# Kernel optimization log

Measured on AMD Instinct MI355X. Metric: run time of the kernel, lower is better.

Reference implementation:

```python
import jax, jax.numpy as jnp
import numpy as np

K = 3          # kernel_size
STRIDE = 1
PAD = 1
DIL = 1


def setup_inputs() -> dict:
    key = jax.random.key(0)
    k1, k2, k3, k4, k5 = jax.random.split(key, 5)
    x = jax.random.normal(k1, (4, 64, 128, 128), jnp.float32)
    weight = jax.random.normal(k2, (64, 64, K, K), jnp.float32) * 0.05   # [O, C, K, K]
    bias = jax.random.normal(k3, (64,), jnp.float32) * 0.05
    # offset conv params: small nonzero so offsets actually exercise bilinear sampling
    offset_w = jax.random.normal(k4, (2 * K * K, 64, K, K), jnp.float32) * 0.01
    offset_b = jax.random.normal(k5, (2 * K * K,), jnp.float32) * 0.1
    return {"x": x, "weight": weight, "bias": bias,
            "offset_w": offset_w, "offset_b": offset_b}


def _conv2d(x, w, b):
    y = jax.lax.conv_general_dilated(
        x, w, window_strides=(STRIDE, STRIDE),
        padding=((PAD, PAD), (PAD, PAD)), rhs_dilation=(DIL, DIL),
        dimension_numbers=("NCHW", "OIHW", "NCHW"))
    return y + b[None, :, None, None]


def _bilinear_sample(img, ys, xs):
    # img: [C, H, W]; ys, xs: [KK, Ho, Wo] float sampling coords
    H, W = img.shape[1], img.shape[2]
    y0 = jnp.floor(ys)
    x0 = jnp.floor(xs)
    y1 = y0 + 1.0
    x1 = x0 + 1.0
    wy1 = ys - y0
    wx1 = xs - x0
    wy0 = 1.0 - wy1
    wx0 = 1.0 - wx1

    def gather(yy, xx):
        valid = (yy >= 0) & (yy <= H - 1) & (xx >= 0) & (xx <= W - 1)
        yi = jnp.clip(yy, 0, H - 1).astype(jnp.int32)
        xi = jnp.clip(xx, 0, W - 1).astype(jnp.int32)
        v = img[:, yi, xi]                     # [C, KK, Ho, Wo]
        return v * valid.astype(img.dtype)

    return (gather(y0, x0) * (wy0 * wx0) + gather(y0, x1) * (wy0 * wx1)
            + gather(y1, x0) * (wy1 * wx0) + gather(y1, x1) * (wy1 * wx1))


def reference(x, weight, bias, offset_w, offset_b):
    B, C, H, W = x.shape
    KK = K * K
    # offsets: [B, 2*K*K, Ho, Wo], per-location (dy, dx) for each kernel tap
    offset = _conv2d(x, offset_w, offset_b)
    Ho, Wo = offset.shape[2], offset.shape[3]
    off = offset.reshape(B, KK, 2, Ho, Wo)
    dy, dx = off[:, :, 0], off[:, :, 1]        # [B, KK, Ho, Wo]

    ki, kj = jnp.meshgrid(jnp.arange(K), jnp.arange(K), indexing="ij")
    ki = ki.reshape(KK).astype(x.dtype)
    kj = kj.reshape(KK).astype(x.dtype)
    oy = (jnp.arange(Ho) * STRIDE - PAD).astype(x.dtype)
    ox = (jnp.arange(Wo) * STRIDE - PAD).astype(x.dtype)
    base_y = oy[None, :, None] + (ki * DIL)[:, None, None]   # [KK, Ho, 1]
    base_x = ox[None, None, :] + (kj * DIL)[:, None, None]   # [KK, 1, Wo]
    ys = base_y[None] + dy                                   # [B, KK, Ho, Wo]
    xs = base_x[None] + dx

    # sampled: [B, C, KK, Ho, Wo]
    sampled = jax.vmap(_bilinear_sample)(x, ys, xs)
    w = weight.reshape(weight.shape[0], C, KK)
    out = jnp.einsum("bckhw,ock->bohw", sampled, w) + bias[None, :, None, None]
    return out
```

## Files before the change

kernel.cpp:

```cpp
#include <hip/hip_runtime.h>
#include <hip/hip_bf16.h>

#define B_ 4
#define C_ 64
#define H_ 128
#define W_ 128
#define HW_ (H_ * W_)
#define OCH_ 18

typedef __attribute__((ext_vector_type(8))) short short8;
typedef __attribute__((ext_vector_type(16))) float f32x16;

#define W2B_ELEMS (9 * 2 * 4 * 64 * 8)
#define W2A_ELEMS (36 * 64 * 8)

#define PSTRIDE_B (6 * 128 * 16 + 16)
#define SMEM_BYTES (8 * PSTRIDE_B)

__device__ __forceinline__ unsigned short f2bf(float f) {
  union { float f; unsigned u; } v; v.f = f;
  unsigned r = v.u + 0x7FFFu + ((v.u >> 16) & 1u);
  return (unsigned short)(r >> 16);
}
__device__ __forceinline__ float bf2f(unsigned short h) {
  union { unsigned u; float f; } v; v.u = ((unsigned)h) << 16;
  return v.f;
}
__device__ __forceinline__ unsigned short f2bfh(float f) {
  __hip_bfloat16 h = __float2bfloat16(f);
  return *reinterpret_cast<unsigned short*>(&h);
}
__device__ __forceinline__ int swz256(int x) { return (x & 7) * 32 + (x >> 3); }
__device__ __forceinline__ int swe(int row, int col) {
  int e = (row << 7) + col;
  e ^= (col >> 3) & 7;
  return e << 4;
}

__global__ __launch_bounds__(256) void pack_w_only(
    const float* __restrict__ wmain, const float* __restrict__ offw,
    unsigned short* __restrict__ ws_u) {
  int idx = blockIdx.x * 256 + threadIdx.x;
  if (idx < W2B_ELEMS) {
    int i = idx & 7, lane = (idx >> 3) & 63, s = (idx >> 9) & 3;
    int mq = (idx >> 11) & 1, t = idx >> 12;
    int o = mq * 32 + (lane & 31);
    int c = 16 * s + (lane >> 5) * 8 + i;
    ws_u[idx] = f2bf(wmain[(o * 64 + c) * 9 + t]);
  } else if (idx < W2B_ELEMS + W2A_ELEMS) {
    int j = idx - W2B_ELEMS;
    int i = j & 7, lane = (j >> 3) & 63, s = j >> 9;
    int kg = 16 * s + (lane >> 5) * 8 + i;
    int t = kg >> 6, c = kg & 63, oc = lane & 31;
    ws_u[idx] = (oc < OCH_) ? f2bf(offw[(oc * 64 + c) * 9 + t]) : (unsigned short)0;
  }
}

template<int KI, int KJ>
__device__ __forceinline__ void tap_full(
    float dy, float dx, int ho, int ho0, int px, int lane, int b,
    const char* __restrict__ win, const float* __restrict__ x,
    const unsigned short* __restrict__ wt2,
    f32x16& acc0, f32x16& acc1) {
  const float ys = (float)(ho - 1 + KI) + dy;
  const float xs = (float)(px - 1 + KJ) + dx;
  const float y0f = floorf(ys), x0f = floorf(xs);
  const int y0 = (int)y0f, x0 = (int)x0f;
  const int y1 = y0 + 1, x1 = x0 + 1;
  const float wy1 = ys - y0f, wx1 = xs - x0f;
  const float wy0 = 1.f - wy1, wx0 = 1.f - wx1;
  const bool vy0 = (unsigned)y0 < (unsigned)H_, vy1 = (unsigned)y1 < (unsigned)H_;
  const bool vx0 = (unsigned)x0 < (unsigned)W_, vx1 = (unsigned)x1 < (unsigned)W_;
  const float g00 = (vy0 && vx0) ? wy0 * wx0 : 0.f;
  const float g01 = (vy0 && vx1) ? wy0 * wx1 : 0.f;
  const float g10 = (vy1 && vx0) ? wy1 * wx0 : 0.f;
  const float g11 = (vy1 && vx1) ? wy1 * wx1 : 0.f;
  const int yc0 = min(max(y0, 0), H_ - 1), yc1 = min(max(y1, 0), H_ - 1);
  const int xc0 = min(max(x0, 0), W_ - 1), xc1 = min(max(x1, 0), W_ - 1);
  const int rr0 = yc0 - ho0 + 2, rr1 = yc1 - ho0 + 2;
  const bool in = ((unsigned)rr0 < 6u) & ((unsigned)rr1 < 6u);
  const int laneh = lane >> 5;

  if (__builtin_expect(__any(!in), 0)) {
    const float* xb = x + (size_t)b * C_ * HW_;
    #pragma unroll 1
    for (int ss = 0; ss < 4; ++ss) {
      short8 bf;
      #pragma unroll
      for (int i = 0; i < 8; ++i) {
        const float* img = xb + (size_t)((2 * ss + laneh) * 8 + i) * HW_;
        float v = g00 * img[yc0 * W_ + xc0] + g01 * img[yc0 * W_ + xc1]
                + g10 * img[yc1 * W_ + xc0] + g11 * img[yc1 * W_ + xc1];
        bf[i] = (short)f2bfh(v);
      }
      const short8 a0 = *(const short8*)&wt2[(ss * 64 + lane) * 8];
      const short8 a1 = *(const short8*)&wt2[((4 + ss) * 64 + lane) * 8];
      acc0 = __builtin_amdgcn_mfma_f32_32x32x16_bf16(a0, bf, acc0, 0, 0, 0);
      acc1 = __builtin_amdgcn_mfma_f32_32x32x16_bf16(a1, bf, acc1, 0, 0, 0);
    }
    return;
  }

  const int u00 = swe(rr0, xc0), u01 = swe(rr0, xc1);
  const int u10 = swe(rr1, xc0), u11 = swe(rr1, xc1);
  #pragma unroll
  for (int ss = 0; ss < 4; ++ss) {
    const char* pb = win + (2 * ss + laneh) * PSTRIDE_B;
    short8 c00 = *(const short8*)(pb + u00);
    short8 c01 = *(const short8*)(pb + u01);
    short8 c10 = *(const short8*)(pb + u10);
    short8 c11 = *(const short8*)(pb + u11);
    short8 bf;
    #pragma unroll
    for (int i = 0; i < 8; ++i) {
      float v = g00 * bf2f((unsigned short)c00[i]) + g01 * bf2f((unsigned short)c01[i])
              + g10 * bf2f((unsigned short)c10[i]) + g11 * bf2f((unsigned short)c11[i]);
      bf[i] = (short)f2bfh(v);
    }
    const short8 a0 = *(const short8*)&wt2[(ss * 64 + lane) * 8];
    const short8 a1 = *(const short8*)&wt2[((4 + ss) * 64 + lane) * 8];
    acc0 = __builtin_amdgcn_mfma_f32_32x32x16_bf16(a0, bf, acc0, 0, 0, 0);
    acc1 = __builtin_amdgcn_mfma_f32_32x32x16_bf16(a1, bf, acc1, 0, 0, 0);
  }
}

#define EXT(T)                                                                          \
  {                                                                                     \
    constexpr int ocy = 2 * (T), ocx = 2 * (T) + 1;                                     \
    constexpr int ry = (ocy & 3) + 4 * (ocy >> 3), hy = (ocy >> 2) & 1;                 \
    constexpr int rx = (ocx & 3) + 4 * (ocx >> 3), hx = (ocx >> 2) & 1;                 \
    dys[T] = __shfl(pacc[ry], (lane & 31) + (hy << 5)) + ob[ocy];                       \
    dxs[T] = __shfl(pacc[rx], (lane & 31) + (hx << 5)) + ob[ocx];                       \
  }

#define TAP(KI, KJ)                                                                     \
  tap_full<KI, KJ>(dys[(KI) * 3 + (KJ)], dxs[(KI) * 3 + (KJ)], ho, ho0, px, lane, b,    \
                   smem, x, w2b + ((KI) * 3 + (KJ)) * 4096, acc0, acc1)

__global__ __launch_bounds__(512, 2) void deform_fused6(
    const float* __restrict__ x, const float* __restrict__ bias,
    const float* __restrict__ ob, const unsigned short* __restrict__ w2b,
    const unsigned short* __restrict__ w2a, float* __restrict__ out) {
  const int blk = swz256(blockIdx.x);
  const int ho0 = (blk & 63) * 2;
  const int b   = blk >> 6;
  const int tid = threadIdx.x;
  const int lane = tid & 63;
  const int wave = tid >> 6;
  const int r_off = wave >> 2;
  const int pair  = wave & 3;
  const int ho = ho0 + r_off;
  const int px = pair * 32 + (lane & 31);
  const int laneh = lane >> 5;

  __shared__ __align__(16) char smem[SMEM_BYTES];

  const float* xb = x + (size_t)b * C_ * HW_;
  #pragma unroll
  for (int it = 0; it < 12; ++it) {
    const int u = tid + it * 512;
    const int cp = u / 192;
    const int rem = u - cp * 192;
    const int row = rem >> 5;
    const int col4 = rem & 31;
    const int srow = min(H_ - 1, max(0, ho0 - 2 + row));
    const int c0 = cp * 2;
    union { float4 v; float f[4]; } fa, fb;
    fa.v = *(const float4*)&xb[(size_t)c0 * HW_ + srow * W_ + col4 * 4];
    fb.v = *(const float4*)&xb[(size_t)(c0 + 1) * HW_ + srow * W_ + col4 * 4];
    char* pl = smem + (cp >> 2) * PSTRIDE_B + ((c0 & 7) << 1);
    #pragma unroll
    for (int j = 0; j < 4; ++j) {
      unsigned pk = (unsigned)f2bfh(fa.f[j]) | ((unsigned)f2bfh(fb.f[j]) << 16);
      *(unsigned*)(pl + swe(row, col4 * 4 + j)) = pk;
    }
  }
  __syncthreads();

  f32x16 pacc_a, pacc_b;
  #pragma unroll
  for (int r = 0; r < 16; ++r) { pacc_a[r] = 0.f; pacc_b[r] = 0.f; }

  #pragma unroll
  for (int s = 0; s < 36; ++s) {
    const int t  = s >> 2;
    const int ki = t / 3, kj = t - 3 * (t / 3);
    const int row = ho - 1 + ki;
    const int col = px - 1 + kj;
    short8 bfr = {0, 0, 0, 0, 0, 0, 0, 0};
    if (((unsigned)row < (unsigned)H_) && ((unsigned)col < (unsigned)W_))
      bfr = *(const short8*)(smem + ((s & 3) * 2 + laneh) * PSTRIDE_B
                             + swe(ki + 1 + r_off, col));
    const short8 afr = *(const short8*)&w2a[((size_t)s * 64 + lane) * 8];
    if (s & 1)
      pacc_b = __builtin_amdgcn_mfma_f32_32x32x16_bf16(afr, bfr, pacc_b, 0, 0, 0);
    else
      pacc_a = __builtin_amdgcn_mfma_f32_32x32x16_bf16(afr, bfr, pacc_a, 0, 0, 0);
  }

  f32x16 pacc;
  #pragma unroll
  for (int r = 0; r < 16; ++r) pacc[r] = pacc_a[r] + pacc_b[r];

  float dys[9], dxs[9];
  EXT(0); EXT(1); EXT(2); EXT(3); EXT(4); EXT(5); EXT(6); EXT(7); EXT(8);

  f32x16 acc0, acc1;
  #pragma unroll
  for (int r = 0; r < 16; ++r) { acc0[r] = 0.f; acc1[r] = 0.f; }

  TAP(0, 0); TAP(0, 1); TAP(0, 2);
  TAP(1, 0); TAP(1, 1); TAP(1, 2);
  TAP(2, 0); TAP(2, 1); TAP(2, 2);

  #pragma unroll
  for (int reg = 0; reg < 16; ++reg) {
    const int row = (reg & 3) + 8 * (reg >> 2) + 4 * laneh;
    out[((b * 64 + row)      * H_ + ho) * W_ + px] = acc0[reg] + bias[row];
    out[((b * 64 + 32 + row) * H_ + ho) * W_ + px] = acc1[reg] + bias[32 + row];
  }
}

extern "C" void kernel_launch(void* const* d_in, const int* in_sizes, int n_in,
                              void* d_out, int out_size, void* d_ws, size_t ws_size,
                              hipStream_t stream) {
  const float* x    = (const float*)d_in[0];
  const float* wt   = (const float*)d_in[1];
  const float* bias = (const float*)d_in[2];
  const float* ow   = (const float*)d_in[3];
  const float* ob   = (const float*)d_in[4];
  float* out = (float*)d_out;

  unsigned short* ws_u = (unsigned short*)d_ws;
  unsigned short* w2b  = ws_u;
  unsigned short* w2a  = ws_u + W2B_ELEMS;

  const int pack_blocks = (W2B_ELEMS + W2A_ELEMS + 255) / 256;
  pack_w_only<<<pack_blocks, 256, 0, stream>>>(wt, ow, ws_u);

  deform_fused6<<<B_ * (H_ / 2), 512, 0, stream>>>(x, bias, ob, w2b, w2a, out);
}
```

Baseline: 40.47 us.

## Drop LDS swizzle, stage 8-channel vectors per thread, batch gather loads, pack bilinear math

```diff
diff --git a/kernel.cpp b/kernel.cpp
--- a/kernel.cpp
+++ b/kernel.cpp
@@ -10,6 +10,7 @@
 
 typedef __attribute__((ext_vector_type(8))) short short8;
 typedef __attribute__((ext_vector_type(16))) float f32x16;
+typedef __attribute__((ext_vector_type(2))) float float2v;
 
 #define W2B_ELEMS (9 * 2 * 4 * 64 * 8)
 #define W2A_ELEMS (36 * 64 * 8)
@@ -30,12 +31,10 @@
   __hip_bfloat16 h = __float2bfloat16(f);
   return *reinterpret_cast<unsigned short*>(&h);
 }
+__device__ __forceinline__ float uaf(unsigned u) {
+  union { unsigned u; float f; } v; v.u = u; return v.f;
+}
 __device__ __forceinline__ int swz256(int x) { return (x & 7) * 32 + (x >> 3); }
-__device__ __forceinline__ int swe(int row, int col) {
-  int e = (row << 7) + col;
-  e ^= (col >> 3) & 7;
-  return e << 4;
-}
 
 __global__ __launch_bounds__(256) void pack_w_only(
     const float* __restrict__ wmain, const float* __restrict__ offw,
@@ -101,21 +100,35 @@
     return;
   }
 
-  const int u00 = swe(rr0, xc0), u01 = swe(rr0, xc1);
-  const int u10 = swe(rr1, xc0), u11 = swe(rr1, xc1);
+  const int u00 = ((rr0 << 7) + xc0) << 4, u01 = ((rr0 << 7) + xc1) << 4;
+  const int u10 = ((rr1 << 7) + xc0) << 4, u11 = ((rr1 << 7) + xc1) << 4;
+
+  short8 c00[4], c01[4], c10[4], c11[4];
   #pragma unroll
   for (int ss = 0; ss < 4; ++ss) {
     const char* pb = win + (2 * ss + laneh) * PSTRIDE_B;
-    short8 c00 = *(const short8*)(pb + u00);
-    short8 c01 = *(const short8*)(pb + u01);
-    short8 c10 = *(const short8*)(pb + u10);
-    short8 c11 = *(const short8*)(pb + u11);
+    c00[ss] = *(const short8*)(pb + u00);
+    c01[ss] = *(const short8*)(pb + u01);
+    c10[ss] = *(const short8*)(pb + u10);
+    c11[ss] = *(const short8*)(pb + u11);
+  }
+
+  #pragma unroll
+  for (int ss = 0; ss < 4; ++ss) {
     short8 bf;
     #pragma unroll
-    for (int i = 0; i < 8; ++i) {
-      float v = g00 * bf2f((unsigned short)c00[i]) + g01 * bf2f((unsigned short)c01[i])
-              + g10 * bf2f((unsigned short)c10[i]) + g11 * bf2f((unsigned short)c11[i]);
-      bf[i] = (short)f2bfh(v);
+    for (int d = 0; d < 4; ++d) {
+      const unsigned w00 = ((const unsigned*)&c00[ss])[d];
+      const unsigned w01 = ((const unsigned*)&c01[ss])[d];
+      const unsigned w10 = ((const unsigned*)&c10[ss])[d];
+      const unsigned w11 = ((const unsigned*)&c11[ss])[d];
+      float2v p00, p01, p10, p11;
+      p00.x = uaf(w00 << 16); p00.y = uaf(w00 & 0xFFFF0000u);
+      p01.x = uaf(w01 << 16); p01.y = uaf(w01 & 0xFFFF0000u);
+      p10.x = uaf(w10 << 16); p10.y = uaf(w10 & 0xFFFF0000u);
+      p11.x = uaf(w11 << 16); p11.y = uaf(w11 & 0xFFFF0000u);
+      float2v v = p00 * g00 + p01 * g01 + p10 * g10 + p11 * g11;
+      ((unsigned*)&bf)[d] = (unsigned)f2bfh(v.x) | ((unsigned)f2bfh(v.y) << 16);
     }
     const short8 a0 = *(const short8*)&wt2[(ss * 64 + lane) * 8];
     const short8 a1 = *(const short8*)&wt2[((4 + ss) * 64 + lane) * 8];
@@ -137,7 +150,7 @@
   tap_full<KI, KJ>(dys[(KI) * 3 + (KJ)], dxs[(KI) * 3 + (KJ)], ho, ho0, px, lane, b,    \
                    smem, x, w2b + ((KI) * 3 + (KJ)) * 4096, acc0, acc1)
 
-__global__ __launch_bounds__(512, 2) void deform_fused6(
+__global__ __launch_bounds__(512, 2) void deform_fused7(
     const float* __restrict__ x, const float* __restrict__ bias,
     const float* __restrict__ ob, const unsigned short* __restrict__ w2b,
     const unsigned short* __restrict__ w2a, float* __restrict__ out) {
@@ -157,22 +170,24 @@
 
   const float* xb = x + (size_t)b * C_ * HW_;
   #pragma unroll
-  for (int it = 0; it < 12; ++it) {
+  for (int it = 0; it < 3; ++it) {
     const int u = tid + it * 512;
-    const int cp = u / 192;
-    const int rem = u - cp * 192;
-    const int row = rem >> 5;
-    const int col4 = rem & 31;
+    const int row  = u >> 8;
+    const int p    = (u >> 5) & 7;
+    const int col4 = u & 31;
     const int srow = min(H_ - 1, max(0, ho0 - 2 + row));
-    const int c0 = cp * 2;
-    union { float4 v; float f[4]; } fa, fb;
-    fa.v = *(const float4*)&xb[(size_t)c0 * HW_ + srow * W_ + col4 * 4];
-    fb.v = *(const float4*)&xb[(size_t)(c0 + 1) * HW_ + srow * W_ + col4 * 4];
-    char* pl = smem + (cp >> 2) * PSTRIDE_B + ((c0 & 7) << 1);
+    const float* bp = xb + (size_t)(p * 8) * HW_ + srow * W_ + col4 * 4;
+    float4 f[8];
+    #pragma unroll
+    for (int i = 0; i < 8; ++i) f[i] = *(const float4*)(bp + (size_t)i * HW_);
+    char* outb = smem + p * PSTRIDE_B + (((row << 7) + col4 * 4) << 4);
     #pragma unroll
     for (int j = 0; j < 4; ++j) {
-      unsigned pk = (unsigned)f2bfh(fa.f[j]) | ((unsigned)f2bfh(fb.f[j]) << 16);
-      *(unsigned*)(pl + swe(row, col4 * 4 + j)) = pk;
+      short8 v;
+      #pragma unroll
+      for (int i = 0; i < 8; ++i)
+        v[i] = (short)f2bfh(reinterpret_cast<const float*>(&f[i])[j]);
+      *(short8*)(outb + j * 16) = v;
     }
   }
   __syncthreads();
@@ -190,7 +205,7 @@
     short8 bfr = {0, 0, 0, 0, 0, 0, 0, 0};
     if (((unsigned)row < (unsigned)H_) && ((unsigned)col < (unsigned)W_))
       bfr = *(const short8*)(smem + ((s & 3) * 2 + laneh) * PSTRIDE_B
-                             + swe(ki + 1 + r_off, col));
+                             + ((((ki + 1 + r_off) << 7) + col) << 4));
     const short8 afr = *(const short8*)&w2a[((size_t)s * 64 + lane) * 8];
     if (s & 1)
       pacc_b = __builtin_amdgcn_mfma_f32_32x32x16_bf16(afr, bfr, pacc_b, 0, 0, 0);
@@ -238,5 +253,5 @@
   const int pack_blocks = (W2B_ELEMS + W2A_ELEMS + 255) / 256;
   pack_w_only<<<pack_blocks, 256, 0, stream>>>(wt, ow, ws_u);
 
-  deform_fused6<<<B_ * (H_ / 2), 512, 0, stream>>>(x, bias, ob, w2b, w2a, out);
-}
+  deform_fused7<<<B_ * (H_ / 2), 512, 0, stream>>>(x, bias, ob, w2b, w2a, out);
+}
```

Measured after the change: 40.38 us. No clear change (-0.2%).
